# Performance work log

Hardware: AMD Instinct MI355X
Metric: run time of the kernel (lower is better)

## Reference

```python
import jax, jax.numpy as jnp
import numpy as np

TEMPERATURE = 0.5


def setup_inputs() -> dict:
    key = jax.random.key(0)
    k1, k2 = jax.random.split(key)
    N, D = 4096, 256
    emb_i = jax.random.normal(k1, (N, D), dtype=jnp.float32)
    emb_j = jax.random.normal(k2, (N, D), dtype=jnp.float32)
    return {"emb_i": emb_i, "emb_j": emb_j, "batch_size": N}


def reference(emb_i, emb_j, batch_size):
    N = batch_size
    # L2-normalize each embedding row (F.normalize eps=1e-12)
    def l2n(x):
        return x / jnp.maximum(jnp.linalg.norm(x, axis=1, keepdims=True), 1e-12)
    reps = jnp.concatenate([l2n(emb_i), l2n(emb_j)], axis=0)  # [2N, D]
    # cosine similarity of normalized vectors == dot product
    logits = (reps @ reps.T) / TEMPERATURE                    # [2N, 2N]
    twoN = 2 * N
    # denominator excludes only the self term k != i (stable logsumexp)
    diag_mask = jnp.eye(twoN, dtype=bool)
    masked = jnp.where(diag_mask, -jnp.inf, logits)
    log_denom = jax.nn.logsumexp(masked, axis=1)              # [2N]
    # positive pair for row i is (i+N) mod 2N
    idx = jnp.arange(twoN)
    pos = logits[idx, (idx + N) % twoN]                       # [2N]
    # loss = 1/(2N) * sum_i -log(exp(pos_i)/denom_i)
    return jnp.mean(log_denom - pos)
```

## Files before the change

### kernel.cpp

```cpp
#include <hip/hip_runtime.h>
#include <hip/hip_fp8.h>

typedef float f32x4 __attribute__((ext_vector_type(4)));

#define TWO_N 8192
#define NHALF 4096
#define DDIM  256

__device__ __forceinline__ float b2f(unsigned short u) {
    return __uint_as_float(((unsigned int)u) << 16);
}
__device__ __forceinline__ unsigned short f2b(float f) {
    unsigned int u = __float_as_uint(f);
    u += 0x7fffu + ((u >> 16) & 1u);
    return (unsigned short)(u >> 16);
}
__device__ __forceinline__ unsigned char f2e4m3(float f) {
    return (unsigned char)__hip_cvt_float_to_fp8(f, __HIP_SATFINITE, __HIP_E4M3);
}

__device__ __forceinline__ int probe_is_f32(const void* p, int lane) {
    unsigned int u = ((const unsigned int*)p)[lane];
    float lowv = __uint_as_float(u << 16);
    int crazy = !(fabsf(lowv) <= 1024.0f);
    return __ballot(crazy) != 0ull;
}

typedef __attribute__((address_space(1))) const unsigned int guint_t;
typedef __attribute__((address_space(3))) unsigned int luint_t;
__device__ __forceinline__ void gl_lds16(const void* g, void* l) {
    __builtin_amdgcn_global_load_lds((guint_t*)g, (luint_t*)l, 16, 0, 0);
}

__device__ __forceinline__ void ast(float* p, float v) {
    __hip_atomic_store(p, v, __ATOMIC_RELAXED, __HIP_MEMORY_SCOPE_AGENT);
}
__device__ __forceinline__ float ald(const float* p) {
    return __hip_atomic_load(p, __ATOMIC_RELAXED, __HIP_MEMORY_SCOPE_AGENT);
}

__global__ __launch_bounds__(256) void k_norm(const void* __restrict__ ei,
                                              const void* __restrict__ ej,
                                              unsigned char* __restrict__ reps8,
                                              unsigned int* __restrict__ ctr) {
    if (blockIdx.x == 0 && threadIdx.x == 0)
        __hip_atomic_store(ctr, 0u, __ATOMIC_RELAXED, __HIP_MEMORY_SCOPE_AGENT);

    int row  = (blockIdx.x * 256 + threadIdx.x) >> 6;
    int lane = threadIdx.x & 63;
    int isf  = probe_is_f32(ei, lane);
    int first = (row < NHALF);
    int r     = first ? row : row - NHALF;
    float x0, x1, x2, x3;
    if (isf) {
        const float* s = (first ? (const float*)ei : (const float*)ej) + (size_t)r * DDIM;
        float4 v = ((const float4*)s)[lane];
        x0 = v.x; x1 = v.y; x2 = v.z; x3 = v.w;
    } else {
        const unsigned short* s =
            (first ? (const unsigned short*)ei : (const unsigned short*)ej) + (size_t)r * DDIM;
        ushort4 v = ((const ushort4*)s)[lane];
        x0 = b2f(v.x); x1 = b2f(v.y); x2 = b2f(v.z); x3 = b2f(v.w);
    }
    float ss = x0 * x0 + x1 * x1 + x2 * x2 + x3 * x3;
    for (int off = 32; off > 0; off >>= 1) ss += __shfl_xor(ss, off);
    float inv = 1.0f / fmaxf(sqrtf(ss), 1e-12f);
    uchar4 o;
    o.x = f2e4m3(x0 * inv); o.y = f2e4m3(x1 * inv);
    o.z = f2e4m3(x2 * inv); o.w = f2e4m3(x3 * inv);
    ((uchar4*)(reps8 + (size_t)row * DDIM))[lane] = o;
}

__global__ __launch_bounds__(256, 4) void k_main(const unsigned char* __restrict__ R8,
                                                 float* __restrict__ S_part,
                                                 float* __restrict__ pos) {
    __shared__ __align__(16) unsigned char As[8192];
    __shared__ __align__(16) unsigned char Bs[8192];

    int b = (int)blockIdx.x;
    int rb = (int)((129.0f - sqrtf(16641.0f - 8.0f * (float)b)) * 0.5f);
    if (rb > 63) rb = 63;
    while ((129 * (rb + 1) - (rb + 1) * (rb + 1)) / 2 <= b) ++rb;
    while ((129 * rb - rb * rb) / 2 > b) --rb;
    int cb = rb + (b - (129 * rb - rb * rb) / 2);

    const int tid  = threadIdx.x;
    const int wave = tid >> 6;
    const int lane = tid & 63;
    const int quad = lane >> 4;
    const int l16  = lane & 15;
    const int wr   = (wave >> 1) * 64;
    const int wc   = (wave & 1) * 64;
    const int r4   = lane >> 2;
    const int g4   = (lane & 3) ^ ((lane >> 3) & 3);
    const int swr  = (l16 >> 1) & 3;
    const int kc0  = (b >> 3) & 3;

    f32x4 acc[4][4];
#pragma unroll
    for (int r = 0; r < 4; ++r)
#pragma unroll
        for (int c = 0; c < 4; ++c) {
            acc[r][c][0] = 0.0f; acc[r][c][1] = 0.0f;
            acc[r][c][2] = 0.0f; acc[r][c][3] = 0.0f;
        }

    for (int i = 0; i < 4; ++i) {
        const int kc = (kc0 + i) & 3;
        __syncthreads();
#pragma unroll
        for (int t = 0; t < 2; ++t) {
            int u = wave * 2 + t;
            const unsigned char* ga =
                R8 + (size_t)(rb * 128 + u * 16 + r4) * DDIM + kc * 64 + g4 * 16;
            const unsigned char* gb =
                R8 + (size_t)(cb * 128 + u * 16 + r4) * DDIM + kc * 64 + g4 * 16;
            gl_lds16(ga, &As[u * 1024]);
            gl_lds16(gb, &Bs[u * 1024]);
        }
        __syncthreads();

#pragma unroll
        for (int kk = 0; kk < 2; ++kk) {
            long afr[4], bfr[4];
            int q  = kk * 4 + quad;
            int po = ((q >> 1) ^ swr) * 16 + (q & 1) * 8;
#pragma unroll
            for (int r = 0; r < 4; ++r)
                afr[r] = *(const long*)(&As[(wr + r * 16 + l16) * 64 + po]);
#pragma unroll
            for (int c = 0; c < 4; ++c)
                bfr[c] = *(const long*)(&Bs[(wc + c * 16 + l16) * 64 + po]);
#pragma unroll
            for (int r = 0; r < 4; ++r)
#pragma unroll
                for (int c = 0; c < 4; ++c)
                    acc[r][c] = __builtin_amdgcn_mfma_f32_16x16x32_fp8_fp8(
                        afr[r], bfr[c], acc[r][c], 0, 0, 0);
        }
    }

    float col_acc[4] = {0.0f, 0.0f, 0.0f, 0.0f};
#pragma unroll
    for (int r = 0; r < 4; ++r)
#pragma unroll
        for (int j = 0; j < 4; ++j) {
            float s = 0.0f;
#pragma unroll
            for (int c = 0; c < 4; ++c) {
                float e = __expf(fmaf(acc[r][c][j], 2.0f, -2.0f));
                s += e;
                col_acc[c] += e;
            }
            s += __shfl_xor(s, 1);
            s += __shfl_xor(s, 2);
            s += __shfl_xor(s, 4);
            s += __shfl_xor(s, 8);
            if (l16 == 0) {
                int row = rb * 128 + wr + r * 16 + quad * 4 + j;
                S_part[(size_t)(2 * cb + (wave & 1)) * TWO_N + row] = s;
            }
        }
    if (rb != cb) {
#pragma unroll
        for (int c = 0; c < 4; ++c) {
            float s = col_acc[c];
            s += __shfl_xor(s, 16);
            s += __shfl_xor(s, 32);
            if (lane < 16) {
                int row = cb * 128 + wc + c * 16 + lane;
                S_part[(size_t)(2 * rb + (wave >> 1)) * TWO_N + row] = s;
            }
        }
    }
    if (cb == rb + 32 && wr == wc) {
#pragma unroll
        for (int r = 0; r < 4; ++r)
#pragma unroll
            for (int j = 0; j < 4; ++j)
                if (quad * 4 + j == l16)
                    pos[rb * 128 + wr + r * 16 + l16] = 2.0f * acc[r][r][j];
    }
}

__global__ __launch_bounds__(256) void k_rows(const float* __restrict__ S_part,
                                              const float* __restrict__ pos,
                                              float* __restrict__ part_blk,
                                              unsigned int* __restrict__ ctr,
                                              unsigned int* __restrict__ out) {
    __shared__ float red[256];
    __shared__ float red2[4];
    __shared__ unsigned int sdone;
    int tid = threadIdx.x;
    int rr  = tid & 63;
    int cg  = tid >> 6;
    int row = blockIdx.x * 64 + rr;
    float s = 0.0f;
#pragma unroll 8
    for (int c = cg * 32; c < cg * 32 + 32; ++c)
        s += S_part[(size_t)c * TWO_N + row];
    red[tid] = s;
    __syncthreads();
    if (tid < 64) {
        float total = red[tid] + red[tid + 64] + red[tid + 128] + red[tid + 192];
        float p = (row < NHALF) ? pos[row] : pos[row - NHALF];
        float part = 2.0f + logf(total - 1.0f) - p;
        for (int off = 32; off > 0; off >>= 1) part += __shfl_xor(part, off);
        if (tid == 0) ast(&part_blk[blockIdx.x], part);
    }
    __syncthreads();
    if (tid == 0)
        sdone = __hip_atomic_fetch_add(ctr, 1u, __ATOMIC_RELAXED,
                                       __HIP_MEMORY_SCOPE_AGENT);
    __syncthreads();
    if (sdone == 127u) {
        float v = (tid < 128) ? ald(&part_blk[tid]) : 0.0f;
        for (int off = 32; off > 0; off >>= 1) v += __shfl_xor(v, off);
        if ((tid & 63) == 0) red2[tid >> 6] = v;
        __syncthreads();
        if (tid == 0) {
            float L = (red2[0] + red2[1] + red2[2] + red2[3]) / 8192.0f;
            unsigned int bb = (unsigned int)f2b(L);
            out[0] = (bb << 16) | bb;
        }
    }
}

extern "C" void kernel_launch(void* const* d_in, const int* in_sizes, int n_in,
                              void* d_out, int out_size, void* d_ws, size_t ws_size,
                              hipStream_t stream) {
    (void)in_sizes; (void)n_in; (void)out_size; (void)ws_size;
    const void* ei = d_in[0];
    const void* ej = d_in[1];
    char* ws = (char*)d_ws;

    float*          pos      = (float*)(ws);
    float*          part_blk = (float*)(ws + 16384);
    unsigned int*   ctr      = (unsigned int*)(ws + 17408);
    unsigned char*  reps8    = (unsigned char*)(ws + 49152);
    float*          S_part   = (float*)(ws + 4243456);

    k_norm<<<2048, 256, 0, stream>>>(ei, ej, reps8, ctr);
    k_main<<<2080, 256, 0, stream>>>(reps8, S_part, pos);
    k_rows<<<128,  256, 0, stream>>>(S_part, pos, part_blk, ctr, (unsigned int*)d_out);
}
```

Baseline: 94.42 us.

## Load full K=256 tiles into LDS at once, dropping the K-chunk loop

Each 128x128 block now loads the whole 256-byte fp8 row slices of A and B into 64 KB of LDS in a single pass with one barrier, instead of four 64-wide K chunks each bracketed by two barriers. The XOR swizzle is widened to 16-byte groups across 256-byte rows to avoid bank conflicts. The aim is to remove repeated synchronisation and issue all global-to-LDS loads up front. In exchange the per-block LDS footprint grows from 16 KB to 64 KB and the launch-bounds occupancy hint is dropped, so fewer blocks can reside on each CU.

New measurement: 101.4 us. 7.4% more time.

```diff
diff --git a/kernel.cpp b/kernel.cpp
--- a/kernel.cpp
+++ b/kernel.cpp
@@ -71,11 +71,11 @@
     ((uchar4*)(reps8 + (size_t)row * DDIM))[lane] = o;
 }
 
-__global__ __launch_bounds__(256, 4) void k_main(const unsigned char* __restrict__ R8,
-                                                 float* __restrict__ S_part,
-                                                 float* __restrict__ pos) {
-    __shared__ __align__(16) unsigned char As[8192];
-    __shared__ __align__(16) unsigned char Bs[8192];
+__global__ __launch_bounds__(256) void k_main(const unsigned char* __restrict__ R8,
+                                              float* __restrict__ S_part,
+                                              float* __restrict__ pos) {
+    __shared__ __align__(16) unsigned char As[32768];
+    __shared__ __align__(16) unsigned char Bs[32768];
 
     int b = (int)blockIdx.x;
     int rb = (int)((129.0f - sqrtf(16641.0f - 8.0f * (float)b)) * 0.5f);
@@ -91,10 +91,18 @@
     const int l16  = lane & 15;
     const int wr   = (wave >> 1) * 64;
     const int wc   = (wave & 1) * 64;
-    const int r4   = lane >> 2;
-    const int g4   = (lane & 3) ^ ((lane >> 3) & 3);
-    const int swr  = (l16 >> 1) & 3;
-    const int kc0  = (b >> 3) & 3;
+    const int lr4  = lane >> 4;
+    const int lc   = lane & 15;
+
+#pragma unroll
+    for (int t = 0; t < 8; ++t) {
+        int g  = wave * 8 + t;
+        int ra = g * 4 + lr4;
+        int cg = lc ^ (ra & 7);
+        gl_lds16(R8 + (size_t)(rb * 128 + ra) * DDIM + cg * 16, &As[g * 1024]);
+        gl_lds16(R8 + (size_t)(cb * 128 + ra) * DDIM + cg * 16, &Bs[g * 1024]);
+    }
+    __syncthreads();
 
     f32x4 acc[4][4];
 #pragma unroll
@@ -105,39 +113,25 @@
             acc[r][c][2] = 0.0f; acc[r][c][3] = 0.0f;
         }
 
-    for (int i = 0; i < 4; ++i) {
-        const int kc = (kc0 + i) & 3;
-        __syncthreads();
-#pragma unroll
-        for (int t = 0; t < 2; ++t) {
-            int u = wave * 2 + t;
-            const unsigned char* ga =
-                R8 + (size_t)(rb * 128 + u * 16 + r4) * DDIM + kc * 64 + g4 * 16;
-            const unsigned char* gb =
-                R8 + (size_t)(cb * 128 + u * 16 + r4) * DDIM + kc * 64 + g4 * 16;
-            gl_lds16(ga, &As[u * 1024]);
-            gl_lds16(gb, &Bs[u * 1024]);
-        }
-        __syncthreads();
-
-#pragma unroll
-        for (int kk = 0; kk < 2; ++kk) {
-            long afr[4], bfr[4];
-            int q  = kk * 4 + quad;
-            int po = ((q >> 1) ^ swr) * 16 + (q & 1) * 8;
-#pragma unroll
-            for (int r = 0; r < 4; ++r)
-                afr[r] = *(const long*)(&As[(wr + r * 16 + l16) * 64 + po]);
+    const int swz  = l16 & 7;
+    const int off8 = (quad & 1) * 8;
+#pragma unroll
+    for (int s = 0; s < 8; ++s) {
+        const int c16 = s * 2 + (quad >> 1);
+        const int po  = (c16 ^ swz) * 16 + off8;
+        long afr[4], bfr[4];
+#pragma unroll
+        for (int r = 0; r < 4; ++r)
+            afr[r] = *(const long*)(&As[(wr + r * 16 + l16) * 256 + po]);
+#pragma unroll
+        for (int c = 0; c < 4; ++c)
+            bfr[c] = *(const long*)(&Bs[(wc + c * 16 + l16) * 256 + po]);
+#pragma unroll
+        for (int r = 0; r < 4; ++r)
 #pragma unroll
             for (int c = 0; c < 4; ++c)
-                bfr[c] = *(const long*)(&Bs[(wc + c * 16 + l16) * 64 + po]);
-#pragma unroll
-            for (int r = 0; r < 4; ++r)
-#pragma unroll
-                for (int c = 0; c < 4; ++c)
-                    acc[r][c] = __builtin_amdgcn_mfma_f32_16x16x32_fp8_fp8(
-                        afr[r], bfr[c], acc[r][c], 0, 0, 0);
-        }
+                acc[r][c] = __builtin_amdgcn_mfma_f32_16x16x32_fp8_fp8(
+                    afr[r], bfr[c], acc[r][c], 0, 0, 0);
     }
 
     float col_acc[4] = {0.0f, 0.0f, 0.0f, 0.0f};
```
